# Performance work log

Hardware: AMD Instinct MI355X
Metric: run time of the kernel (lower is better)

## Reference

```python
import jax, jax.numpy as jnp
import numpy as np

B, T, D, R = 8, 4096, 768, 16
DB = D // 3  # bucket size (d_img = d_sym = 256, d_rf = D - 2*DB = 256)


def setup_inputs() -> dict:
    key = jax.random.key(0)
    ks = jax.random.split(key, 10)
    s = 0.05
    x = jax.random.normal(ks[0], (B, T, D), dtype=jnp.float32)
    # torch nn.Linear stores weight as (out, in); y = x @ W.T + b
    V_w = jax.random.normal(ks[1], (R, D), dtype=jnp.float32) * s
    U_w = jax.random.normal(ks[2], (D, R), dtype=jnp.float32) * s
    E1_w = jax.random.normal(ks[3], (DB, D), dtype=jnp.float32) * s
    E1_b = jnp.zeros((DB,), dtype=jnp.float32)
    E2_w = jax.random.normal(ks[4], (3, DB), dtype=jnp.float32) * s
    E2_b = jnp.zeros((3,), dtype=jnp.float32)
    # a_base init per bucket: img=-0.6, sym=-1.0, rf=-1.6; a_delta init 0 (perturbed so tanh path is exercised)
    a_base = jnp.concatenate([
        jnp.full((DB,), -0.6, dtype=jnp.float32),
        jnp.full((DB,), -1.0, dtype=jnp.float32),
        jnp.full((D - 2 * DB,), -1.6, dtype=jnp.float32),
    ])
    a_delta = jax.random.normal(ks[5], (D,), dtype=jnp.float32) * 0.1
    C_w = jax.random.normal(ks[6], (D, D), dtype=jnp.float32) * s
    G_w = jax.random.normal(ks[7], (D, D), dtype=jnp.float32) * s
    G_b = jnp.zeros((D,), dtype=jnp.float32)
    return {"x": x, "V_w": V_w, "U_w": U_w, "E1_w": E1_w, "E1_b": E1_b,
            "E2_w": E2_w, "E2_b": E2_b, "a_base": a_base, "a_delta": a_delta,
            "C_w": C_w, "G_w": G_w, "G_b": G_b}


def reference(x, V_w, U_w, E1_w, E1_b, E2_w, E2_b, a_base, a_delta, C_w, G_w, G_b):
    d = x.shape[-1]
    db = d // 3
    # Low-rank input projection: Bu = U(V(x))
    Z = jnp.einsum('btd,rd->btr', x, V_w)            # (B,T,R)
    Bu = jnp.einsum('btr,dr->btd', Z, U_w)           # (B,T,D)
    # Evidence scores per timestep (3 clinical buckets)
    h = jax.nn.gelu(jnp.einsum('btd,ed->bte', x, E1_w) + E1_b, approximate=False)
    alpha = jax.nn.sigmoid(jnp.einsum('bte,ce->btc', h, E2_w) + E2_b)  # (B,T,3)
    # Broadcast each bucket's evidence score over its channels
    alpha_rep = jnp.concatenate([
        jnp.broadcast_to(alpha[..., 0:1], alpha.shape[:-1] + (db,)),
        jnp.broadcast_to(alpha[..., 1:2], alpha.shape[:-1] + (db,)),
        jnp.broadcast_to(alpha[..., 2:3], alpha.shape[:-1] + (d - 2 * db,)),
    ], axis=-1)                                       # (B,T,D)
    a_eff = a_base + alpha_rep * jnp.tanh(a_delta)    # (B,T,D)
    lam = jnp.exp(-jax.nn.softplus(-a_eff))           # (B,T,D), in (0,1)
    # Diagonal linear recurrence s_t = lam_t * s_{t-1} + Bu_t  (scan over time)
    def step(s, inp):
        l_t, bu_t = inp
        s = l_t * s + bu_t
        return s, s
    s0 = jnp.zeros(x.shape[:1] + x.shape[2:], dtype=x.dtype)  # (B,D)
    _, S = jax.lax.scan(step, s0, (jnp.swapaxes(lam, 0, 1), jnp.swapaxes(Bu, 0, 1)))
    S = jnp.swapaxes(S, 0, 1)                         # (B,T,D)
    y = jnp.einsum('btd,od->bto', S, C_w)
    gate = jax.nn.sigmoid(jnp.einsum('btd,od->bto', x, G_w) + G_b)
    y = jax.nn.gelu(y, approximate=False) * gate
    return x + y  # dropout is identity in eval mode
```

## Files before the change

### kernel.cpp

```cpp
#include <hip/hip_runtime.h>
#include <hip/hip_bf16.h>
#include <math.h>

#define B_   8
#define T_   4096
#define D_   768
#define R_   16
#define DB_  256
#define N_   (B_ * T_)
#define NC_  64
#define L_   (T_ / NC_)
#define NKS_ (D_ / 32)
#define BUF_ 12288

typedef __attribute__((ext_vector_type(8))) short bf16x8;
typedef __attribute__((ext_vector_type(4))) float f32x4;

__device__ __forceinline__ float gelu_exact(float x) {
    return 0.5f * x * (1.0f + erff(x * 0.70710678118654752f));
}
__device__ __forceinline__ float sigmoidf_(float x) {
    return 1.0f / (1.0f + expf(-x));
}
__device__ __forceinline__ float bf2f(unsigned short u) {
    return __uint_as_float(((unsigned)u) << 16);
}
__device__ __forceinline__ unsigned short f2bf(float f) {
    __hip_bfloat16 h = __float2bfloat16(f);
    return *(unsigned short*)&h;
}
__device__ __forceinline__ bf16x8 pack8(float4 a, float4 b) {
    bf16x8 r;
    r[0] = (short)f2bf(a.x); r[1] = (short)f2bf(a.y);
    r[2] = (short)f2bf(a.z); r[3] = (short)f2bf(a.w);
    r[4] = (short)f2bf(b.x); r[5] = (short)f2bf(b.y);
    r[6] = (short)f2bf(b.z); r[7] = (short)f2bf(b.w);
    return r;
}

__device__ __forceinline__ void gload16(const unsigned short* g, unsigned short* l) {
    __builtin_amdgcn_global_load_lds(
        (const __attribute__((address_space(1))) unsigned int*)(const void*)g,
        (__attribute__((address_space(3))) unsigned int*)(void*)l,
        16, 0, 0);
}

__device__ __forceinline__ bf16x8 frag_read(const unsigned short* lds, int row, int lq) {
    int q = lq ^ ((row >> 1) & 3);
    return *(const bf16x8*)(lds + row * 32 + q * 8);
}

__device__ __forceinline__ void tile_decode(int nwg, int ncol, int& rowt, int& colt) {
    int bid = blockIdx.x;
    int cpx = nwg >> 3;
    int swz = (bid & 7) * cpx + (bid >> 3);
    colt = swz % ncol;
    rowt = swz / ncol;
}

__device__ __forceinline__ void stage_a(const unsigned short* src, int row0, int k0,
                                        unsigned short* lds, int w, int l) {
#pragma unroll
    for (int j = 0; j < 2; ++j) {
        int i = ((w * 2 + j) << 6) + l;
        int row = i >> 2, q = i & 3;
        int qs = q ^ ((row >> 1) & 3);
        gload16(src + (size_t)(row0 + row) * D_ + k0 + qs * 8, lds + ((w * 2 + j) << 9));
    }
}
__device__ __forceinline__ void stage_b(const unsigned short* src, int col0, int k0,
                                        unsigned short* lds, int w, int l) {
    int i = (w << 6) + l;
    int row = i >> 2, q = i & 3;
    int qs = q ^ ((row >> 1) & 3);
    gload16(src + (size_t)(col0 + row) * D_ + k0 + qs * 8, lds + (w << 9));
}

__device__ __forceinline__ void tile_mfma44(const unsigned short* la, const unsigned short* lb,
                                            int wrow, int wcol, int lr, int lq,
                                            f32x4 acc[4][4]) {
    bf16x8 a[4], b[4];
#pragma unroll
    for (int m = 0; m < 4; m++) a[m] = frag_read(la, wrow + m * 16 + lr, lq);
#pragma unroll
    for (int n = 0; n < 4; n++) b[n] = frag_read(lb, wcol + n * 16 + lr, lq);
    __builtin_amdgcn_s_setprio(1);
#pragma unroll
    for (int m = 0; m < 4; m++)
#pragma unroll
        for (int n = 0; n < 4; n++)
            acc[m][n] = __builtin_amdgcn_mfma_f32_16x16x32_bf16(a[m], b[n], acc[m][n], 0, 0, 0);
    __builtin_amdgcn_s_setprio(0);
}

__device__ __forceinline__ void prologueF(const unsigned short* __restrict__ A,
                                          const unsigned short* __restrict__ Bm,
                                          int row0, int col0,
                                          unsigned short* lds, int w, int l) {
    stage_a(A,  row0, 0,  lds,                w, l);
    stage_b(Bm, col0, 0,  lds + 8192,         w, l);
    stage_a(A,  row0, 32, lds + BUF_,         w, l);
    stage_b(Bm, col0, 32, lds + BUF_ + 8192,  w, l);
}

template <bool DO_PROLOGUE>
__device__ __forceinline__ void kloopF(const unsigned short* __restrict__ A,
                                       const unsigned short* __restrict__ Bm,
                                       int row0, int col0,
                                       unsigned short* lds,
                                       int w, int l, f32x4 acc[4][4]) {
    const int lr = l & 15, lq = l >> 4;
    const int wrow = (w >> 1) * 64, wcol = (w & 1) * 64;

    if (DO_PROLOGUE) prologueF(A, Bm, row0, col0, lds, w, l);

#pragma unroll 3
    for (int t = 0; t < NKS_ - 2; ++t) {
        asm volatile("s_waitcnt vmcnt(3)" ::: "memory");
        __builtin_amdgcn_s_barrier();
        __builtin_amdgcn_sched_barrier(0);
        unsigned short* bn = lds + ((t + 2) % 3) * BUF_;
        stage_a(A,  row0, (t + 2) * 32, bn,        w, l);
        stage_b(Bm, col0, (t + 2) * 32, bn + 8192, w, l);
        unsigned short* bc = lds + (t % 3) * BUF_;
        tile_mfma44(bc, bc + 8192, wrow, wcol, lr, lq, acc);
    }
    asm volatile("s_waitcnt vmcnt(3)" ::: "memory");
    __builtin_amdgcn_s_barrier();
    __builtin_amdgcn_sched_barrier(0);
    {
        unsigned short* bc = lds + ((NKS_ - 2) % 3) * BUF_;
        tile_mfma44(bc, bc + 8192, wrow, wcol, lr, lq, acc);
    }
    asm volatile("s_waitcnt vmcnt(0)" ::: "memory");
    __builtin_amdgcn_s_barrier();
    __builtin_amdgcn_sched_barrier(0);
    {
        unsigned short* bc = lds + ((NKS_ - 1) % 3) * BUF_;
        tile_mfma44(bc, bc + 8192, wrow, wcol, lr, lq, acc);
    }
}

__global__ __launch_bounds__(512, 2)
void gemm_fused_out(const unsigned short* __restrict__ Xb,
                    const unsigned short* __restrict__ Gwb,
                    const unsigned short* __restrict__ Sb,
                    const unsigned short* __restrict__ Cwb,
                    const float* __restrict__ Gbias,
                    float* __restrict__ out) {
    __shared__ unsigned short lds[3 * BUF_];
    const int t = threadIdx.x, l = t & 63, w = t >> 6;
    int rowt, colt;
    tile_decode(768, 6, rowt, colt);
    const int row0 = rowt * 256, col0 = colt * 128;
    const int lr = l & 15, lq = l >> 4;
    const int wrow = (w >> 1) * 64, wcol = (w & 1) * 64;

    float gb[4];
#pragma unroll
    for (int n = 0; n < 4; n++) gb[n] = Gbias[col0 + wcol + n * 16 + lr];

    f32x4 acc[4][4] = {};
    kloopF<true>(Xb, Gwb, row0, col0, lds, w, l, acc);

    prologueF(Sb, Cwb, row0, col0, lds, w, l);

    unsigned int gp[4][4][2];
#pragma unroll
    for (int m = 0; m < 4; m++)
#pragma unroll
        for (int n = 0; n < 4; n++) {
            gp[m][n][0] = (unsigned)f2bf(sigmoidf_(acc[m][n][0] + gb[n]))
                        | ((unsigned)f2bf(sigmoidf_(acc[m][n][1] + gb[n])) << 16);
            gp[m][n][1] = (unsigned)f2bf(sigmoidf_(acc[m][n][2] + gb[n]))
                        | ((unsigned)f2bf(sigmoidf_(acc[m][n][3] + gb[n])) << 16);
            acc[m][n] = (f32x4){0.f, 0.f, 0.f, 0.f};
        }

    kloopF<false>(Sb, Cwb, row0, col0, lds, w, l, acc);

#pragma unroll
    for (int m = 0; m < 4; m++)
#pragma unroll
        for (int n = 0; n < 4; n++) {
            int col = col0 + wcol + n * 16 + lr;
#pragma unroll
            for (int r = 0; r < 4; r++) {
                int row = row0 + wrow + m * 16 + lq * 4 + r;
                size_t o = (size_t)row * D_ + col;
                float g = bf2f((unsigned short)(gp[m][n][r >> 1] >> ((r & 1) * 16)));
                out[o] = bf2f(Xb[o]) + gelu_exact(acc[m][n][r]) * g;
            }
        }
}

__global__ __launch_bounds__(512, 2)
void gemm_e1_alpha(const unsigned short* __restrict__ Xb,
                   const unsigned short* __restrict__ Wb,
                   const float* __restrict__ bias,
                   const float* __restrict__ E2w,
                   float* __restrict__ alpha_acc) {
    __shared__ unsigned short lds[3 * BUF_];
    const int t = threadIdx.x, l = t & 63, w = t >> 6;
    int rowt, colt;
    tile_decode(256, 2, rowt, colt);
    const int row0 = rowt * 256, col0 = colt * 128;
    const int lr = l & 15, lq = l >> 4;
    const int wrow = (w >> 1) * 64, wcol = (w & 1) * 64;
    f32x4 acc[4][4] = {};
    kloopF<true>(Xb, Wb, row0, col0, lds, w, l, acc);

    float bia[4], e2v[3][4];
#pragma unroll
    for (int n = 0; n < 4; n++) {
        int col = col0 + wcol + n * 16 + lr;
        bia[n] = bias[col];
#pragma unroll
        for (int c = 0; c < 3; c++) e2v[c][n] = E2w[c * DB_ + col];
    }
#pragma unroll
    for (int m = 0; m < 4; m++)
#pragma unroll
        for (int r = 0; r < 4; r++) {
            float p0 = 0.f, p1 = 0.f, p2 = 0.f;
#pragma unroll
            for (int n = 0; n < 4; n++) {
                float h = gelu_exact(acc[m][n][r] + bia[n]);
                p0 = fmaf(h, e2v[0][n], p0);
                p1 = fmaf(h, e2v[1][n], p1);
                p2 = fmaf(h, e2v[2][n], p2);
            }
#pragma unroll
            for (int s = 1; s < 16; s <<= 1) {
                p0 += __shfl_xor(p0, s);
                p1 += __shfl_xor(p1, s);
                p2 += __shfl_xor(p2, s);
            }
            if (lr == 0) {
                int row = row0 + wrow + m * 16 + lq * 4 + r;
                atomicAdd(&alpha_acc[(size_t)row * 3 + 0], p0);
                atomicAdd(&alpha_acc[(size_t)row * 3 + 1], p1);
                atomicAdd(&alpha_acc[(size_t)row * 3 + 2], p2);
            }
        }
}

__global__ __launch_bounds__(256)
void cvtz_kernel(const float* __restrict__ X, const float* __restrict__ Vw,
                 unsigned short* __restrict__ Xb, float* __restrict__ Z) {
    const int t = threadIdx.x, l = t & 63, w = t >> 6;
    const int lr = l & 15, lq = l >> 4;
    const int tok0 = (blockIdx.x * 4 + w) * 16;
    const float* xrow = X  + (size_t)(tok0 + lr) * D_;
    const float* vrow = Vw + (size_t)lr * D_;
    f32x4 acc = {};
#pragma unroll 4
    for (int k0 = 0; k0 < D_; k0 += 32) {
        int k = k0 + lq * 8;
        float4 xa = *(const float4*)&xrow[k];
        float4 xb = *(const float4*)&xrow[k + 4];
        float4 va = *(const float4*)&vrow[k];
        float4 vb = *(const float4*)&vrow[k + 4];
        bf16x8 xf = pack8(xa, xb);
        bf16x8 vf = pack8(va, vb);
        *(bf16x8*)&Xb[(size_t)(tok0 + lr) * D_ + k] = xf;
        acc = __builtin_amdgcn_mfma_f32_16x16x32_bf16(xf, vf, acc, 0, 0, 0);
    }
#pragma unroll
    for (int rr = 0; rr < 4; rr++)
        Z[(size_t)(tok0 + lq * 4 + rr) * R_ + lr] = acc[rr];
}

#define SEG_E1  (DB_ * D_ / 4)
#define SEG_W   (D_ * D_ / 4)
#define SEG_Z   (N_ * 3 / 4)
#define SEG_TOT (SEG_E1 + 2 * SEG_W + SEG_Z + 192)

__global__ void setup_all(const float* __restrict__ E1_w, const float* __restrict__ C_w,
                          const float* __restrict__ G_w, const float* __restrict__ a_delta,
                          unsigned short* __restrict__ E1b, unsigned short* __restrict__ Cwb,
                          unsigned short* __restrict__ Gwb, float* __restrict__ al_acc,
                          float* __restrict__ tanhd) {
    int i = blockIdx.x * 256 + threadIdx.x;
    if (i < SEG_E1) {
        float4 v = ((const float4*)E1_w)[i];
        ((ushort4*)E1b)[i] = make_ushort4(f2bf(v.x), f2bf(v.y), f2bf(v.z), f2bf(v.w));
    } else if (i < SEG_E1 + SEG_W) {
        int j = i - SEG_E1;
        float4 v = ((const float4*)C_w)[j];
        ((ushort4*)Cwb)[j] = make_ushort4(f2bf(v.x), f2bf(v.y), f2bf(v.z), f2bf(v.w));
    } else if (i < SEG_E1 + 2 * SEG_W) {
        int j = i - SEG_E1 - SEG_W;
        float4 v = ((const float4*)G_w)[j];
        ((ushort4*)Gwb)[j] = make_ushort4(f2bf(v.x), f2bf(v.y), f2bf(v.z), f2bf(v.w));
    } else if (i < SEG_E1 + 2 * SEG_W + SEG_Z) {
        int j = i - SEG_E1 - 2 * SEG_W;
        ((float4*)al_acc)[j] = make_float4(0.f, 0.f, 0.f, 0.f);
    } else if (i < SEG_TOT) {
        int j = (i - SEG_E1 - 2 * SEG_W - SEG_Z) * 4;
        tanhd[j + 0] = tanhf(a_delta[j + 0]);
        tanhd[j + 1] = tanhf(a_delta[j + 1]);
        tanhd[j + 2] = tanhf(a_delta[j + 2]);
        tanhd[j + 3] = tanhf(a_delta[j + 3]);
    }
}

__device__ __forceinline__ void load_chunk_lds(const float* __restrict__ Z,
                                               const float* __restrict__ al_acc,
                                               const float* __restrict__ E2b,
                                               int tok0, int t,
                                               float* Zs, float* als) {
#pragma unroll
    for (int i = t; i < L_ * R_ / 4; i += 192)
        *(float4*)&Zs[i * 4] = *(const float4*)&Z[(size_t)tok0 * R_ + i * 4];
    als[t] = sigmoidf_(al_acc[(size_t)tok0 * 3 + t] + E2b[t % 3]);
}

__device__ __forceinline__ float dot16(const float* zrow, const float4* u) {
    float4 z0 = *(const float4*)&zrow[0],  z1 = *(const float4*)&zrow[4];
    float4 z2 = *(const float4*)&zrow[8],  z3 = *(const float4*)&zrow[12];
    return z0.x*u[0].x + z0.y*u[0].y + z0.z*u[0].z + z0.w*u[0].w
         + z1.x*u[1].x + z1.y*u[1].y + z1.z*u[1].z + z1.w*u[1].w
         + z2.x*u[2].x + z2.y*u[2].y + z2.z*u[2].z + z2.w*u[2].w
         + z3.x*u[3].x + z3.y*u[3].y + z3.z*u[3].z + z3.w*u[3].w;
}

__global__ __launch_bounds__(192)
void scan_pass1(const float* __restrict__ Z, const float* __restrict__ al_acc,
                const float* __restrict__ E2b,
                const float* __restrict__ Uw, const float* __restrict__ a_base,
                const float* __restrict__ tanhd,
                float* __restrict__ Aagg, float* __restrict__ Send) {
    __shared__ float Zs[L_ * R_];
    __shared__ float als[L_ * 3];
    const int t = threadIdx.x;
    const int c = blockIdx.x & (NC_ - 1);
    const int b = blockIdx.x >> 6;
    const int tok0 = b * T_ + c * L_;
    const int d0 = t * 4;
    const int buck = d0 >> 8;
    load_chunk_lds(Z, al_acc, E2b, tok0, t, Zs, als);

    float4 u[4][4];
#pragma unroll
    for (int j = 0; j < 4; j++)
#pragma unroll
        for (int q = 0; q < 4; q++)
            u[j][q] = *(const float4*)&Uw[(size_t)(d0 + j) * R_ + q * 4];
    float4 ab = *(const float4*)&a_base[d0];
    float4 td = *(const float4*)&tanhd[d0];
    float abv[4] = {ab.x, ab.y, ab.z, ab.w};
    float tdv[4] = {td.x, td.y, td.z, td.w};
    __syncthreads();

    float a[4] = {1.f, 1.f, 1.f, 1.f}, s[4] = {};
    for (int i = 0; i < L_; i++) {
        float av = als[i * 3 + buck];
#pragma unroll
        for (int j = 0; j < 4; j++) {
            float lam = sigmoidf_(fmaf(av, tdv[j], abv[j]));
            float bu  = dot16(&Zs[i * R_], u[j]);
            a[j] *= lam;
            s[j] = fmaf(lam, s[j], bu);
        }
    }
    size_t o = ((size_t)(b * NC_ + c)) * D_ + d0;
    *(float4*)&Aagg[o] = make_float4(a[0], a[1], a[2], a[3]);
    *(float4*)&Send[o] = make_float4(s[0], s[1], s[2], s[3]);
}

__global__ __launch_bounds__(192)
void scan_pass3(const float* __restrict__ Z, const float* __restrict__ al_acc,
                const float* __restrict__ E2b,
                const float* __restrict__ Uw, const float* __restrict__ a_base,
                const float* __restrict__ tanhd,
                const float* __restrict__ Aagg, const float* __restrict__ Send,
                unsigned short* __restrict__ Sout) {
    __shared__ float Zs[L_ * R_];
    __shared__ float als[L_ * 3];
    const int t = threadIdx.x;
    const int c = blockIdx.x & (NC_ - 1);
    const int b = blockIdx.x >> 6;
    const int tok0 = b * T_ + c * L_;
    const int d0 = t * 4;
    const int buck = d0 >> 8;
    load_chunk_lds(Z, al_acc, E2b, tok0, t, Zs, als);

    float4 u[4][4];
#pragma unroll
    for (int j = 0; j < 4; j++)
#pragma unroll
        for (int q = 0; q < 4; q++)
            u[j][q] = *(const float4*)&Uw[(size_t)(d0 + j) * R_ + q * 4];
    float4 ab = *(const float4*)&a_base[d0];
    float4 td = *(const float4*)&tanhd[d0];
    float abv[4] = {ab.x, ab.y, ab.z, ab.w};
    float tdv[4] = {td.x, td.y, td.z, td.w};

    float s[4] = {0.f, 0.f, 0.f, 0.f};
#pragma unroll 4
    for (int cc = 0; cc < c; ++cc) {
        size_t o = ((size_t)(b * NC_ + cc)) * D_ + d0;
        float4 a4 = *(const float4*)&Aagg[o];
        float4 s4 = *(const float4*)&Send[o];
        s[0] = fmaf(a4.x, s[0], s4.x);
        s[1] = fmaf(a4.y, s[1], s4.y);
        s[2] = fmaf(a4.z, s[2], s4.z);
        s[3] = fmaf(a4.w, s[3], s4.w);
    }
    __syncthreads();

    for (int i = 0; i < L_; i++) {
        float av = als[i * 3 + buck];
#pragma unroll
        for (int j = 0; j < 4; j++) {
            float lam = sigmoidf_(fmaf(av, tdv[j], abv[j]));
            float bu  = dot16(&Zs[i * R_], u[j]);
            s[j] = fmaf(lam, s[j], bu);
        }
        *(ushort4*)&Sout[(size_t)(tok0 + i) * D_ + d0] =
            make_ushort4(f2bf(s[0]), f2bf(s[1]), f2bf(s[2]), f2bf(s[3]));
    }
}

extern "C" void kernel_launch(void* const* d_in, const int* in_sizes, int n_in,
                              void* d_out, int out_size, void* d_ws, size_t ws_size,
                              hipStream_t stream) {
    const float* x       = (const float*)d_in[0];
    const float* V_w     = (const float*)d_in[1];
    const float* U_w     = (const float*)d_in[2];
    const float* E1_w    = (const float*)d_in[3];
    const float* E1_b    = (const float*)d_in[4];
    const float* E2_w    = (const float*)d_in[5];
    const float* E2_b    = (const float*)d_in[6];
    const float* a_base  = (const float*)d_in[7];
    const float* a_delta = (const float*)d_in[8];
    const float* C_w     = (const float*)d_in[9];
    const float* G_w     = (const float*)d_in[10];
    const float* G_b     = (const float*)d_in[11];
    float* out = (float*)d_out;

    char* p = (char*)d_ws;
    float* Aagg   = (float*)p;          p += (size_t)B_ * NC_ * D_ * 4;
    float* Send   = (float*)p;          p += (size_t)B_ * NC_ * D_ * 4;
    float* tanhd  = (float*)p;          p += (size_t)D_ * 4;
    float* Z      = (float*)p;          p += (size_t)N_ * R_ * 4;
    float* al_acc = (float*)p;          p += (size_t)N_ * 3 * 4;
    unsigned short* x_bf  = (unsigned short*)p; p += (size_t)N_ * D_ * 2;
    unsigned short* S_bf  = (unsigned short*)p; p += (size_t)N_ * D_ * 2;
    unsigned short* E1_bf = (unsigned short*)p; p += (size_t)DB_ * D_ * 2;
    unsigned short* Cw_bf = (unsigned short*)p; p += (size_t)D_ * D_ * 2;
    unsigned short* Gw_bf = (unsigned short*)p; p += (size_t)D_ * D_ * 2;

    setup_all<<<(SEG_TOT + 255) / 256, 256, 0, stream>>>(
        E1_w, C_w, G_w, a_delta, E1_bf, Cw_bf, Gw_bf, al_acc, tanhd);

    cvtz_kernel<<<N_ / 64, 256, 0, stream>>>(x, V_w, x_bf, Z);

    gemm_e1_alpha<<<256, 512, 0, stream>>>(x_bf, E1_bf, E1_b, E2_w, al_acc);

    scan_pass1<<<B_ * NC_, 192, 0, stream>>>(Z, al_acc, E2_b, U_w, a_base, tanhd, Aagg, Send);
    scan_pass3<<<B_ * NC_, 192, 0, stream>>>(Z, al_acc, E2_b, U_w, a_base, tanhd, Aagg, Send, S_bf);

    gemm_fused_out<<<768, 512, 0, stream>>>(x_bf, Gw_bf, S_bf, Cw_bf, G_b, out);
}
```

Measured before the change: 290.6 us.

## Halve E1 GEMM tile height and fold setup kernel into cvtz kernel

The E1/alpha GEMM now uses 128x128 tiles with a dedicated triple-buffered k-loop (2x4 MFMAs per wave), doubling the grid to 512 blocks so more CUs have work on this small GEMM. The separate setup kernel that casts weights to bf16, zeroes the alpha accumulator and computes tanh is merged into cvtz_kernel as a grid-stride tail, which removes one launch. The smaller tiles cost more operand reloads per FLOP, and the merged weight casts now run in the same kernel as the x conversion.

```diff
diff --git a/kernel.cpp b/kernel.cpp
--- a/kernel.cpp
+++ b/kernel.cpp
@@ -11,7 +11,8 @@
 #define NC_  64
 #define L_   (T_ / NC_)
 #define NKS_ (D_ / 32)
-#define BUF_ 12288
+#define BUF_  12288
+#define BUFE_ 8192
 
 typedef __attribute__((ext_vector_type(8))) short bf16x8;
 typedef __attribute__((ext_vector_type(4))) float f32x4;
@@ -194,21 +195,80 @@
         }
 }
 
+__device__ __forceinline__ void stage_e(const unsigned short* __restrict__ A,
+                                        const unsigned short* __restrict__ Bm,
+                                        int row0, int col0, int k0,
+                                        unsigned short* buf, int w, int l) {
+    int i = (w << 6) + l;
+    int row = i >> 2, q = i & 3;
+    int qs = q ^ ((row >> 1) & 3);
+    gload16(A  + (size_t)(row0 + row) * D_ + k0 + qs * 8, buf + (w << 9));
+    gload16(Bm + (size_t)(col0 + row) * D_ + k0 + qs * 8, buf + 4096 + (w << 9));
+}
+
+__device__ __forceinline__ void tile_mfma24(const unsigned short* buf,
+                                            int wrow, int wcol, int lr, int lq,
+                                            f32x4 acc[2][4]) {
+    const unsigned short* la = buf;
+    const unsigned short* lb = buf + 4096;
+    bf16x8 a[2], b[4];
+#pragma unroll
+    for (int m = 0; m < 2; m++) a[m] = frag_read(la, wrow + m * 16 + lr, lq);
+#pragma unroll
+    for (int n = 0; n < 4; n++) b[n] = frag_read(lb, wcol + n * 16 + lr, lq);
+    __builtin_amdgcn_s_setprio(1);
+#pragma unroll
+    for (int m = 0; m < 2; m++)
+#pragma unroll
+        for (int n = 0; n < 4; n++)
+            acc[m][n] = __builtin_amdgcn_mfma_f32_16x16x32_bf16(a[m], b[n], acc[m][n], 0, 0, 0);
+    __builtin_amdgcn_s_setprio(0);
+}
+
+__device__ __forceinline__ void kloopE(const unsigned short* __restrict__ A,
+                                       const unsigned short* __restrict__ Bm,
+                                       int row0, int col0,
+                                       unsigned short* lds,
+                                       int w, int l, f32x4 acc[2][4]) {
+    const int lr = l & 15, lq = l >> 4;
+    const int wrow = (w >> 1) * 32, wcol = (w & 1) * 64;
+
+    stage_e(A, Bm, row0, col0, 0,  lds,         w, l);
+    stage_e(A, Bm, row0, col0, 32, lds + BUFE_, w, l);
+
+#pragma unroll 3
+    for (int t = 0; t < NKS_ - 2; ++t) {
+        asm volatile("s_waitcnt vmcnt(2)" ::: "memory");
+        __builtin_amdgcn_s_barrier();
+        __builtin_amdgcn_sched_barrier(0);
+        stage_e(A, Bm, row0, col0, (t + 2) * 32, lds + ((t + 2) % 3) * BUFE_, w, l);
+        tile_mfma24(lds + (t % 3) * BUFE_, wrow, wcol, lr, lq, acc);
+    }
+    asm volatile("s_waitcnt vmcnt(2)" ::: "memory");
+    __builtin_amdgcn_s_barrier();
+    __builtin_amdgcn_sched_barrier(0);
+    tile_mfma24(lds + ((NKS_ - 2) % 3) * BUFE_, wrow, wcol, lr, lq, acc);
+    asm volatile("s_waitcnt vmcnt(0)" ::: "memory");
+    __builtin_amdgcn_s_barrier();
+    __builtin_amdgcn_sched_barrier(0);
+    tile_mfma24(lds + ((NKS_ - 1) % 3) * BUFE_, wrow, wcol, lr, lq, acc);
+}
+
 __global__ __launch_bounds__(512, 2)
 void gemm_e1_alpha(const unsigned short* __restrict__ Xb,
                    const unsigned short* __restrict__ Wb,
                    const float* __restrict__ bias,
                    const float* __restrict__ E2w,
                    float* __restrict__ alpha_acc) {
-    __shared__ unsigned short lds[3 * BUF_];
+    __shared__ unsigned short lds[3 * BUFE_];
     const int t = threadIdx.x, l = t & 63, w = t >> 6;
     int rowt, colt;
-    tile_decode(256, 2, rowt, colt);
-    const int row0 = rowt * 256, col0 = colt * 128;
+    tile_decode(512, 2, rowt, colt);
+    const int row0 = rowt * 128, col0 = colt * 128;
     const int lr = l & 15, lq = l >> 4;
-    const int wrow = (w >> 1) * 64, wcol = (w & 1) * 64;
-    f32x4 acc[4][4] = {};
-    kloopF<true>(Xb, Wb, row0, col0, lds, w, l, acc);
+    const int wrow = (w >> 1) * 32, wcol = (w & 1) * 64;
+    f32x4 acc[2][4] = {};
+    kloopE(Xb, Wb, row0, col0, lds, w, l, acc);
 
     float bia[4], e2v[3][4];
 #pragma unroll
@@ -219,7 +279,7 @@
         for (int c = 0; c < 3; c++) e2v[c][n] = E2w[c * DB_ + col];
     }
 #pragma unroll
-    for (int m = 0; m < 4; m++)
+    for (int m = 0; m < 2; m++)
 #pragma unroll
         for (int r = 0; r < 4; r++) {
             float p0 = 0.f, p1 = 0.f, p2 = 0.f;
@@ -245,9 +305,19 @@
         }
 }
 
+#define SEG_E1  (DB_ * D_ / 4)
+#define SEG_W   (D_ * D_ / 4)
+#define SEG_Z   (N_ * 3 / 4)
+#define SEG_TOT (SEG_E1 + 2 * SEG_W + SEG_Z + 192)
+
 __global__ __launch_bounds__(256)
 void cvtz_kernel(const float* __restrict__ X, const float* __restrict__ Vw,
-                 unsigned short* __restrict__ Xb, float* __restrict__ Z) {
+                 unsigned short* __restrict__ Xb, float* __restrict__ Z,
+                 const float* __restrict__ E1_w, const float* __restrict__ C_w,
+                 const float* __restrict__ G_w, const float* __restrict__ a_delta,
+                 unsigned short* __restrict__ E1b, unsigned short* __restrict__ Cwb,
+                 unsigned short* __restrict__ Gwb, float* __restrict__ al_acc,
+                 float* __restrict__ tanhd) {
     const int t = threadIdx.x, l = t & 63, w = t >> 6;
     const int lr = l & 15, lq = l >> 4;
     const int tok0 = (blockIdx.x * 4 + w) * 16;
@@ -269,39 +339,29 @@
 #pragma unroll
     for (int rr = 0; rr < 4; rr++)
         Z[(size_t)(tok0 + lq * 4 + rr) * R_ + lr] = acc[rr];
-}
-
-#define SEG_E1  (DB_ * D_ / 4)
-#define SEG_W   (D_ * D_ / 4)
-#define SEG_Z   (N_ * 3 / 4)
-#define SEG_TOT (SEG_E1 + 2 * SEG_W + SEG_Z + 192)
-
-__global__ void setup_all(const float* __restrict__ E1_w, const float* __restrict__ C_w,
-                          const float* __restrict__ G_w, const float* __restrict__ a_delta,
-                          unsigned short* __restrict__ E1b, unsigned short* __restrict__ Cwb,
-                          unsigned short* __restrict__ Gwb, float* __restrict__ al_acc,
-                          float* __restrict__ tanhd) {
-    int i = blockIdx.x * 256 + threadIdx.x;
-    if (i < SEG_E1) {
-        float4 v = ((const float4*)E1_w)[i];
-        ((ushort4*)E1b)[i] = make_ushort4(f2bf(v.x), f2bf(v.y), f2bf(v.z), f2bf(v.w));
-    } else if (i < SEG_E1 + SEG_W) {
-        int j = i - SEG_E1;
-        float4 v = ((const float4*)C_w)[j];
-        ((ushort4*)Cwb)[j] = make_ushort4(f2bf(v.x), f2bf(v.y), f2bf(v.z), f2bf(v.w));
-    } else if (i < SEG_E1 + 2 * SEG_W) {
-        int j = i - SEG_E1 - SEG_W;
-        float4 v = ((const float4*)G_w)[j];
-        ((ushort4*)Gwb)[j] = make_ushort4(f2bf(v.x), f2bf(v.y), f2bf(v.z), f2bf(v.w));
-    } else if (i < SEG_E1 + 2 * SEG_W + SEG_Z) {
-        int j = i - SEG_E1 - 2 * SEG_W;
-        ((float4*)al_acc)[j] = make_float4(0.f, 0.f, 0.f, 0.f);
-    } else if (i < SEG_TOT) {
-        int j = (i - SEG_E1 - 2 * SEG_W - SEG_Z) * 4;
-        tanhd[j + 0] = tanhf(a_delta[j + 0]);
-        tanhd[j + 1] = tanhf(a_delta[j + 1]);
-        tanhd[j + 2] = tanhf(a_delta[j + 2]);
-        tanhd[j + 3] = tanhf(a_delta[j + 3]);
+
+    for (int i = blockIdx.x * 256 + t; i < SEG_TOT; i += 512 * 256) {
+        if (i < SEG_E1) {
+            float4 v = ((const float4*)E1_w)[i];
+            ((ushort4*)E1b)[i] = make_ushort4(f2bf(v.x), f2bf(v.y), f2bf(v.z), f2bf(v.w));
+        } else if (i < SEG_E1 + SEG_W) {
+            int j = i - SEG_E1;
+            float4 v = ((const float4*)C_w)[j];
+            ((ushort4*)Cwb)[j] = make_ushort4(f2bf(v.x), f2bf(v.y), f2bf(v.z), f2bf(v.w));
+        } else if (i < SEG_E1 + 2 * SEG_W) {
+            int j = i - SEG_E1 - SEG_W;
+            float4 v = ((const float4*)G_w)[j];
+            ((ushort4*)Gwb)[j] = make_ushort4(f2bf(v.x), f2bf(v.y), f2bf(v.z), f2bf(v.w));
+        } else if (i < SEG_E1 + 2 * SEG_W + SEG_Z) {
+            int j = i - SEG_E1 - 2 * SEG_W;
+            ((float4*)al_acc)[j] = make_float4(0.f, 0.f, 0.f, 0.f);
+        } else {
+            int j = (i - SEG_E1 - 2 * SEG_W - SEG_Z) * 4;
+            tanhd[j + 0] = tanhf(a_delta[j + 0]);
+            tanhd[j + 1] = tanhf(a_delta[j + 1]);
+            tanhd[j + 2] = tanhf(a_delta[j + 2]);
+            tanhd[j + 3] = tanhf(a_delta[j + 3]);
+        }
     }
 }
 
@@ -452,12 +512,11 @@
     unsigned short* Cw_bf = (unsigned short*)p; p += (size_t)D_ * D_ * 2;
     unsigned short* Gw_bf = (unsigned short*)p; p += (size_t)D_ * D_ * 2;
 
-    setup_all<<<(SEG_TOT + 255) / 256, 256, 0, stream>>>(
-        E1_w, C_w, G_w, a_delta, E1_bf, Cw_bf, Gw_bf, al_acc, tanhd);
-
-    cvtz_kernel<<<N_ / 64, 256, 0, stream>>>(x, V_w, x_bf, Z);
-
-    gemm_e1_alpha<<<256, 512, 0, stream>>>(x_bf, E1_bf, E1_b, E2_w, al_acc);
+    cvtz_kernel<<<N_ / 64, 256, 0, stream>>>(x, V_w, x_bf, Z,
+                                             E1_w, C_w, G_w, a_delta,
+                                             E1_bf, Cw_bf, Gw_bf, al_acc, tanhd);
+
+    gemm_e1_alpha<<<512, 512, 0, stream>>>(x_bf, E1_bf, E1_b, E2_w, al_acc);
 
     scan_pass1<<<B_ * NC_, 192, 0, stream>>>(Z, al_acc, E2_b, U_w, a_base, tanhd, Aagg, Send);
     scan_pass3<<<B_ * NC_, 192, 0, stream>>>(Z, al_acc, E2_b, U_w, a_base, tanhd, Aagg, Send, S_bf);
```

Result: faster. 281.1 us (-3.3%).
